# Kernel tuning notes

Hardware: AMD Instinct MI355X
Metric: run time of the kernel (lower is better)

Reference implementation:

```python
import jax, jax.numpy as jnp
import numpy as np

X_BOUND = (-51.2, 51.2, 0.8)
Y_BOUND = (-51.2, 51.2, 0.8)
Z_BOUND = (-5.0, 3.0, 0.5)
DOWNSAMPLE = 8
NX = int(round((X_BOUND[1] - X_BOUND[0]) / X_BOUND[2]))  # 128
NY = int(round((Y_BOUND[1] - Y_BOUND[0]) / Y_BOUND[2]))  # 128
NZ = int(round((Z_BOUND[1] - Z_BOUND[0]) / Z_BOUND[2]))  # 16


def _frustum():
    # (4, N) homogeneous BEV voxel-center coordinates, N = NX*NY*NZ
    xs = X_BOUND[0] + jnp.arange(NX, dtype=jnp.float32) * X_BOUND[2]
    ys = Y_BOUND[0] + jnp.arange(NY, dtype=jnp.float32) * Y_BOUND[2]
    zs = Z_BOUND[0] + jnp.arange(NZ, dtype=jnp.float32) * Z_BOUND[2]
    pts = jnp.stack(jnp.meshgrid(xs, ys, zs, indexing='ij')).reshape(3, -1)
    return jnp.concatenate([pts, jnp.ones((1, pts.shape[1]), jnp.float32)], axis=0)


def _grid_sample_bilinear(feat, u, v):
    # feat: (B,C,H,W); u,v: (B,N) normalized coords in [-1,1], align_corners=True,
    # padding_mode='zeros'. Returns (B,C,N).
    B, C, H, W = feat.shape
    x = (u + 1.0) * 0.5 * (W - 1)
    y = (v + 1.0) * 0.5 * (H - 1)
    finite = jnp.isfinite(x) & jnp.isfinite(y)
    x = jnp.where(finite, x, -10.0)  # push non-finite coords fully out of range -> 0
    y = jnp.where(finite, y, -10.0)
    x0 = jnp.floor(x); y0 = jnp.floor(y)
    x1 = x0 + 1.0;     y1 = y0 + 1.0
    wx1 = x - x0; wx0 = 1.0 - wx1
    wy1 = y - y0; wy0 = 1.0 - wy1
    feat_flat = feat.reshape(B, C, H * W)

    def corner(xi, yi, w):
        valid = (xi >= 0) & (xi < W) & (yi >= 0) & (yi < H)
        xi_ = jnp.clip(xi, 0, W - 1).astype(jnp.int32)
        yi_ = jnp.clip(yi, 0, H - 1).astype(jnp.int32)
        idx = yi_ * W + xi_  # (B,N)
        vals = jax.vmap(lambda f, i: f[:, i])(feat_flat, idx)  # (B,C,N)
        return vals * (w * valid.astype(feat.dtype))[:, None, :]

    out = (corner(x0, y0, wx0 * wy0) + corner(x1, y0, wx1 * wy0)
           + corner(x0, y1, wx0 * wy1) + corner(x1, y1, wx1 * wy1))
    return jnp.where(jnp.isnan(out), 0.0, out)


def setup_inputs() -> dict:
    key = jax.random.key(0)
    k1, k2, k3, k4 = jax.random.split(key, 4)
    B, C, H, W = 2, 80, 32, 88
    return {
        'img_feats': jax.random.normal(k1, (B, C, H, W), jnp.float32),
        'intrin_mat': jax.random.normal(k2, (B, 1, 4, 4), jnp.float32),
        'extrin_mat': jax.random.normal(k3, (B, 1, 4, 4), jnp.float32),
        'bda_mat': jax.random.normal(k4, (B, 4, 4), jnp.float32),
    }


def reference(img_feats, intrin_mat, extrin_mat, bda_mat):
    B, C, H, W = img_feats.shape
    frustum = _frustum()  # (4, N)
    # intrinsic[..., :2, :] /= downsample_factor
    scale = jnp.array([1.0 / DOWNSAMPLE, 1.0 / DOWNSAMPLE, 1.0], jnp.float32)[:, None]
    intrinsic = intrin_mat[..., :3, :3] * scale          # (B,1,3,3)
    extrinsic = extrin_mat[..., :3, :]                   # (B,1,3,4)
    proj = intrinsic @ extrinsic                         # (B,1,3,4)
    points = jnp.einsum('bij,jn->bin', bda_mat, frustum) # (B,4,N)
    pixels = jnp.einsum('bcij,bjn->bcin', proj, points)  # (B,1,3,N)
    u = pixels[:, 0, 0, :] / pixels[:, 0, 2, :]          # (B,N)
    v = pixels[:, 0, 1, :] / pixels[:, 0, 2, :]
    u = u / W * 2.0 - 1.0
    v = v / H * 2.0 - 1.0
    bev = _grid_sample_bilinear(img_feats, u, v)         # (B,C,N)
    return bev.reshape(B, C, NX, NY, NZ)
```

## Files before the change

kernel.cpp:

```cpp
#include <hip/hip_runtime.h>
#include <hip/hip_bf16.h>
#include <hip/hip_fp16.h>

#define NXg 128
#define NYg 128
#define NZg 16
#define NPT (NXg * NYg * NZg)
#define Hh 32
#define Ww 88
#define Cc 80
#define HWc (Hh * Ww)
#define CSPLIT 4
#define CPB (Cc / CSPLIT)
#define NG (Cc / 4)

__global__ __launch_bounds__(256) void fvt_tohalf(
    const float* __restrict__ feat, unsigned short* __restrict__ featH, int total)
{
    int t = blockIdx.x * 256 + threadIdx.x;
    if (t >= total) return;
    int p = t % HWc; int r = t / HWc;
    int g = r % NG;  int b = r / NG;
    const float* src = feat + ((size_t)(b * Cc + g * 4)) * HWc + p;
    ushort4 px;
    px.x = __half_as_ushort(__float2half(src[0 * HWc]));
    px.y = __half_as_ushort(__float2half(src[1 * HWc]));
    px.z = __half_as_ushort(__float2half(src[2 * HWc]));
    px.w = __half_as_ushort(__float2half(src[3 * HWc]));
    *reinterpret_cast<ushort4*>(featH + (size_t)t * 4) = px;
}

union U2F2 { unsigned u; __half2 h; };
__device__ __forceinline__ float2 cvt2(unsigned u) {
    U2F2 c; c.u = u;
    return __half22float2(c.h);
}

__global__ __launch_bounds__(256) void fvt_kernel(
    const unsigned short* __restrict__ featH,
    const float* __restrict__ intrin,
    const float* __restrict__ extrin,
    const float* __restrict__ bda,
    float* __restrict__ out)
{
    const int b  = blockIdx.y;
    const int cq = blockIdx.z;
    const int t  = blockIdx.x * blockDim.x + threadIdx.x;
    const int n0 = t << 2;
    if (n0 >= NPT) return;

    const float* In = intrin + b * 16;
    const float* Ex = extrin + b * 16;
    const float* Bd = bda    + b * 16;

    float K[3][3];
#pragma unroll
    for (int r = 0; r < 3; ++r)
#pragma unroll
        for (int c = 0; c < 3; ++c)
            K[r][c] = In[r * 4 + c] * (r == 2 ? 1.0f : 0.125f);

    float P[3][4];
#pragma unroll
    for (int r = 0; r < 3; ++r)
#pragma unroll
        for (int c = 0; c < 4; ++c)
            P[r][c] = K[r][0] * Ex[0 * 4 + c] + K[r][1] * Ex[1 * 4 + c] + K[r][2] * Ex[2 * 4 + c];

    float M[3][4];
#pragma unroll
    for (int r = 0; r < 3; ++r)
#pragma unroll
        for (int c = 0; c < 4; ++c)
            M[r][c] = P[r][0] * Bd[0 * 4 + c] + P[r][1] * Bd[1 * 4 + c]
                    + P[r][2] * Bd[2 * 4 + c] + P[r][3] * Bd[3 * 4 + c];

    const int iz0 = n0 & (NZg - 1);
    const int iy  = (n0 >> 4) & (NYg - 1);
    const int ix  = n0 >> 11;
    const float xf = -51.2f + (float)ix * 0.8f;
    const float yf = -51.2f + (float)iy * 0.8f;

    int   off[4][2];
    float wlo[4][2];
    float whi[4][2];
    bool  vj [4];
    bool  anyv = false;

#pragma unroll
    for (int j = 0; j < 4; ++j) {
        const float zf = -5.0f + (float)(iz0 + j) * 0.5f;

        const float px = M[0][0] * xf + M[0][1] * yf + M[0][2] * zf + M[0][3];
        const float py = M[1][0] * xf + M[1][1] * yf + M[1][2] * zf + M[1][3];
        const float pz = M[2][0] * xf + M[2][1] * yf + M[2][2] * zf + M[2][3];

        float u = px / pz;
        float v = py / pz;
        u = u / (float)Ww * 2.0f - 1.0f;
        v = v / (float)Hh * 2.0f - 1.0f;

        float x = (u + 1.0f) * 0.5f * (float)(Ww - 1);
        float y = (v + 1.0f) * 0.5f * (float)(Hh - 1);
        const bool fin = __builtin_isfinite(x) && __builtin_isfinite(y);
        x = fin ? x : -10.0f;
        y = fin ? y : -10.0f;

        const float x0 = floorf(x);
        const float y0 = floorf(y);
        const float x1 = x0 + 1.0f;
        const float y1 = y0 + 1.0f;
        const float wx1 = x - x0, wx0 = 1.0f - wx1;
        const float wy1 = y - y0, wy0 = 1.0f - wy1;

        const bool vx0 = (x0 >= 0.0f) && (x0 < (float)Ww);
        const bool vx1 = (x1 >= 0.0f) && (x1 < (float)Ww);
        const bool vy0 = (y0 >= 0.0f) && (y0 < (float)Hh);
        const bool vy1 = (y1 >= 0.0f) && (y1 < (float)Hh);
        const float w00 = (vx0 && vy0) ? wx0 * wy0 : 0.0f;
        const float w10 = (vx1 && vy0) ? wx1 * wy0 : 0.0f;
        const float w01 = (vx0 && vy1) ? wx0 * wy1 : 0.0f;
        const float w11 = (vx1 && vy1) ? wx1 * wy1 : 0.0f;

        const float xb  = fminf(fmaxf(x0, 0.0f), 86.0f);
        const float y0c = fminf(fmaxf(y0, 0.0f), 31.0f);
        const float y1c = fminf(fmaxf(y1, 0.0f), 31.0f);

        const int xbi = (int)xb;
        off[0 * 0 + j][0] = ((int)y0c * Ww + xbi) * 4;
        off[j][1]         = ((int)y1c * Ww + xbi) * 4;

        const float lo_is_x0 = (x0 == xb) ? 1.0f : 0.0f;
        const float lo_is_x1 = (x1 == xb) ? 1.0f : 0.0f;
        const float hi_is_x0 = (x0 == xb + 1.0f) ? 1.0f : 0.0f;
        const float hi_is_x1 = (x1 == xb + 1.0f) ? 1.0f : 0.0f;
        wlo[j][0] = lo_is_x0 * w00 + lo_is_x1 * w10;
        whi[j][0] = hi_is_x0 * w00 + hi_is_x1 * w10;
        wlo[j][1] = lo_is_x0 * w01 + lo_is_x1 * w11;
        whi[j][1] = hi_is_x0 * w01 + hi_is_x1 * w11;

        const float wsum = w00 + w10 + w01 + w11;
        vj[j] = wsum > 0.0f;
        anyv |= vj[j];
    }

    float* ob = out + ((size_t)b * Cc + cq * CPB) * (size_t)NPT + n0;

    if (!anyv) {
        const float4 z4 = make_float4(0.0f, 0.0f, 0.0f, 0.0f);
#pragma unroll
        for (int q = 0; q < CPB; ++q)
            *reinterpret_cast<float4*>(ob + (size_t)q * NPT) = z4;
        return;
    }

    const unsigned short* fb = featH + ((size_t)b * NG + cq * (CPB / 4)) * (size_t)(HWc * 4);

#pragma unroll 2
    for (int cg = 0; cg < CPB / 4; ++cg) {
        const unsigned short* fg = fb + (size_t)cg * (HWc * 4);
        float acc[4][4];
#pragma unroll
        for (int cc = 0; cc < 4; ++cc)
#pragma unroll
            for (int j = 0; j < 4; ++j) acc[cc][j] = 0.0f;

#pragma unroll
        for (int j = 0; j < 4; ++j) {
            if (vj[j]) {
#pragma unroll
                for (int k = 0; k < 2; ++k) {
                    const uint4 raw = *reinterpret_cast<const uint4*>(fg + off[j][k]);
                    const float wl = wlo[j][k];
                    const float wh = whi[j][k];
                    const float2 lo01 = cvt2(raw.x);
                    const float2 lo23 = cvt2(raw.y);
                    const float2 hi01 = cvt2(raw.z);
                    const float2 hi23 = cvt2(raw.w);
                    acc[0][j] = fmaf(wl, lo01.x, fmaf(wh, hi01.x, acc[0][j]));
                    acc[1][j] = fmaf(wl, lo01.y, fmaf(wh, hi01.y, acc[1][j]));
                    acc[2][j] = fmaf(wl, lo23.x, fmaf(wh, hi23.x, acc[2][j]));
                    acc[3][j] = fmaf(wl, lo23.y, fmaf(wh, hi23.y, acc[3][j]));
                }
            }
        }
#pragma unroll
        for (int cc = 0; cc < 4; ++cc) {
            *reinterpret_cast<float4*>(ob + (size_t)(cg * 4 + cc) * NPT) =
                make_float4(acc[cc][0], acc[cc][1], acc[cc][2], acc[cc][3]);
        }
    }
}

extern "C" void kernel_launch(void* const* d_in, const int* in_sizes, int n_in,
                              void* d_out, int out_size, void* d_ws, size_t ws_size,
                              hipStream_t stream) {
    const float* feat   = (const float*)d_in[0];
    const float* intrin = (const float*)d_in[1];
    const float* extrin = (const float*)d_in[2];
    const float* bda    = (const float*)d_in[3];
    float* out = (float*)d_out;
    unsigned short* featH = (unsigned short*)d_ws;

    const int B = in_sizes[0] / (Cc * HWc);
    const int total = B * NG * HWc;

    fvt_tohalf<<<(total + 255) / 256, 256, 0, stream>>>(feat, featH, total);

    dim3 block(256);
    dim3 grid(NPT / 4 / 256, B, CSPLIT);
    fvt_kernel<<<grid, block, 0, stream>>>(featH, intrin, extrin, bda, out);
}
```

Measured before the change: 41.05 us.

## Stage per-channel-group feature slices in LDS and gather from shared memory

Pads each 4-channel half-precision feature slice to 3072 pixels and has every block cooperatively copy the slice into LDS before each channel-group iteration. The bilinear gathers then read LDS instead of global/L2. The channel split drops from 4 to 2 and launch bounds request higher occupancy. The early-out zero path for fully invalid threads is removed, so every block now pays the slice loads and barriers. It also adds two __syncthreads per channel group.

Measured after the change: 42.20 us. 2.8% more time.

```diff
diff --git a/kernel.cpp b/kernel.cpp
--- a/kernel.cpp
+++ b/kernel.cpp
@@ -10,23 +10,28 @@
 #define Ww 88
 #define Cc 80
 #define HWc (Hh * Ww)
-#define CSPLIT 4
+#define PPAD 3072
+#define CSPLIT 2
 #define CPB (Cc / CSPLIT)
 #define NG (Cc / 4)
+#define NCG (CPB / 4)
+#define SLICE_U4 (PPAD / 2)
 
 __global__ __launch_bounds__(256) void fvt_tohalf(
     const float* __restrict__ feat, unsigned short* __restrict__ featH, int total)
 {
     int t = blockIdx.x * 256 + threadIdx.x;
     if (t >= total) return;
-    int p = t % HWc; int r = t / HWc;
-    int g = r % NG;  int b = r / NG;
-    const float* src = feat + ((size_t)(b * Cc + g * 4)) * HWc + p;
-    ushort4 px;
-    px.x = __half_as_ushort(__float2half(src[0 * HWc]));
-    px.y = __half_as_ushort(__float2half(src[1 * HWc]));
-    px.z = __half_as_ushort(__float2half(src[2 * HWc]));
-    px.w = __half_as_ushort(__float2half(src[3 * HWc]));
+    int p = t % PPAD; int r = t / PPAD;
+    int g = r % NG;   int b = r / NG;
+    ushort4 px = make_ushort4(0, 0, 0, 0);
+    if (p < HWc) {
+        const float* src = feat + ((size_t)(b * Cc + g * 4)) * HWc + p;
+        px.x = __half_as_ushort(__float2half(src[0 * HWc]));
+        px.y = __half_as_ushort(__float2half(src[1 * HWc]));
+        px.z = __half_as_ushort(__float2half(src[2 * HWc]));
+        px.w = __half_as_ushort(__float2half(src[3 * HWc]));
+    }
     *reinterpret_cast<ushort4*>(featH + (size_t)t * 4) = px;
 }
 
@@ -36,18 +41,21 @@
     return __half22float2(c.h);
 }
 
-__global__ __launch_bounds__(256) void fvt_kernel(
+__global__ __launch_bounds__(256, 4) void fvt_kernel(
     const unsigned short* __restrict__ featH,
     const float* __restrict__ intrin,
     const float* __restrict__ extrin,
     const float* __restrict__ bda,
     float* __restrict__ out)
 {
-    const int b  = blockIdx.y;
-    const int cq = blockIdx.z;
-    const int t  = blockIdx.x * blockDim.x + threadIdx.x;
-    const int n0 = t << 2;
-    if (n0 >= NPT) return;
+    __shared__ uint4 sl4[SLICE_U4];
+    const uint2* sl2 = reinterpret_cast<const uint2*>(sl4);
+
+    const int b   = blockIdx.y;
+    const int cq  = blockIdx.z;
+    const int tid = threadIdx.x;
+    const int t   = blockIdx.x * blockDim.x + tid;
+    const int n0  = t << 2;
 
     const float* In = intrin + b * 16;
     const float* Ex = extrin + b * 16;
@@ -81,11 +89,10 @@
     const float xf = -51.2f + (float)ix * 0.8f;
     const float yf = -51.2f + (float)iy * 0.8f;
 
-    int   off[4][2];
+    int   pix[4][2];
     float wlo[4][2];
     float whi[4][2];
     bool  vj [4];
-    bool  anyv = false;
 
 #pragma unroll
     for (int j = 0; j < 4; ++j) {
@@ -127,8 +134,8 @@
         const float y1c = fminf(fmaxf(y1, 0.0f), 31.0f);
 
         const int xbi = (int)xb;
-        off[0 * 0 + j][0] = ((int)y0c * Ww + xbi) * 4;
-        off[j][1]         = ((int)y1c * Ww + xbi) * 4;
+        pix[j][0] = (int)y0c * Ww + xbi;
+        pix[j][1] = (int)y1c * Ww + xbi;
 
         const float lo_is_x0 = (x0 == xb) ? 1.0f : 0.0f;
         const float lo_is_x1 = (x1 == xb) ? 1.0f : 0.0f;
@@ -139,26 +146,32 @@
         wlo[j][1] = lo_is_x0 * w01 + lo_is_x1 * w11;
         whi[j][1] = hi_is_x0 * w01 + hi_is_x1 * w11;
 
-        const float wsum = w00 + w10 + w01 + w11;
-        vj[j] = wsum > 0.0f;
-        anyv |= vj[j];
+        vj[j] = (w00 + w10 + w01 + w11) > 0.0f;
     }
 
     float* ob = out + ((size_t)b * Cc + cq * CPB) * (size_t)NPT + n0;
-
-    if (!anyv) {
-        const float4 z4 = make_float4(0.0f, 0.0f, 0.0f, 0.0f);
-#pragma unroll
-        for (int q = 0; q < CPB; ++q)
-            *reinterpret_cast<float4*>(ob + (size_t)q * NPT) = z4;
-        return;
-    }
-
-    const unsigned short* fb = featH + ((size_t)b * NG + cq * (CPB / 4)) * (size_t)(HWc * 4);
-
-#pragma unroll 2
-    for (int cg = 0; cg < CPB / 4; ++cg) {
-        const unsigned short* fg = fb + (size_t)cg * (HWc * 4);
+    const uint4* fbase = reinterpret_cast<const uint4*>(featH)
+                       + ((size_t)b * NG + cq * NCG) * SLICE_U4;
+
+    for (int cg = 0; cg < NCG; ++cg) {
+        __syncthreads();
+        {
+            const uint4* src = fbase + (size_t)cg * SLICE_U4;
+            uint4 v0 = src[tid];
+            uint4 v1 = src[tid + 256];
+            uint4 v2 = src[tid + 512];
+            uint4 v3 = src[tid + 768];
+            uint4 v4 = src[tid + 1024];
+            uint4 v5 = src[tid + 1280];
+            sl4[tid]        = v0;
+            sl4[tid + 256]  = v1;
+            sl4[tid + 512]  = v2;
+            sl4[tid + 768]  = v3;
+            sl4[tid + 1024] = v4;
+            sl4[tid + 1280] = v5;
+        }
+        __syncthreads();
+
         float acc[4][4];
 #pragma unroll
         for (int cc = 0; cc < 4; ++cc)
@@ -170,13 +183,15 @@
             if (vj[j]) {
 #pragma unroll
                 for (int k = 0; k < 2; ++k) {
-                    const uint4 raw = *reinterpret_cast<const uint4*>(fg + off[j][k]);
+                    const int p = pix[j][k];
+                    const uint2 lo = sl2[p];
+                    const uint2 hi = sl2[p + 1];
                     const float wl = wlo[j][k];
                     const float wh = whi[j][k];
-                    const float2 lo01 = cvt2(raw.x);
-                    const float2 lo23 = cvt2(raw.y);
-                    const float2 hi01 = cvt2(raw.z);
-                    const float2 hi23 = cvt2(raw.w);
+                    const float2 lo01 = cvt2(lo.x);
+                    const float2 lo23 = cvt2(lo.y);
+                    const float2 hi01 = cvt2(hi.x);
+                    const float2 hi23 = cvt2(hi.y);
                     acc[0][j] = fmaf(wl, lo01.x, fmaf(wh, hi01.x, acc[0][j]));
                     acc[1][j] = fmaf(wl, lo01.y, fmaf(wh, hi01.y, acc[1][j]));
                     acc[2][j] = fmaf(wl, lo23.x, fmaf(wh, hi23.x, acc[2][j]));
@@ -203,7 +218,7 @@
     unsigned short* featH = (unsigned short*)d_ws;
 
     const int B = in_sizes[0] / (Cc * HWc);
-    const int total = B * NG * HWc;
+    const int total = B * NG * PPAD;
 
     fvt_tohalf<<<(total + 255) / 256, 256, 0, stream>>>(feat, featH, total);
 
```
